# Kernel optimization log

Hardware: AMD Instinct MI355X
Metric: run time of the kernel (lower is better)

## Reference

```python
import jax, jax.numpy as jnp
import numpy as np
import math
from jax import lax

L = 30      # seq length (DyConv(30,30); fcblock in_dim 420 = 14*30)
D = 14      # d_model / channels
H = 8       # n_heads
E = D // H  # d_keys per head = 1 (torch integer division)
DK = H * E  # inner attention dim = 8
DFF = 50
TOPK = int(math.log(L))  # factor=1 -> 3
MA = 25     # Autoformer series_decomp moving-average kernel
EPS = 1e-5
B = 65536


def layer_norm(x, g, b):
    m = x.mean(-1, keepdims=True)
    v = ((x - m) ** 2).mean(-1, keepdims=True)
    return (x - m) / jnp.sqrt(v + EPS) * g + b


def series_decomp(x):
    # x: (B, L, D). Replicate-pad then moving average (kernel MA, stride 1).
    p = (MA - 1) // 2
    xp = jnp.concatenate([jnp.repeat(x[:, :1], p, axis=1), x, jnp.repeat(x[:, -1:], p, axis=1)], axis=1)
    cs = jnp.cumsum(xp, axis=1)
    cs = jnp.concatenate([jnp.zeros_like(cs[:, :1]), cs], axis=1)
    mean = (cs[:, MA:] - cs[:, :-MA]) / MA  # (B, L, D)
    return x - mean, mean


def _forward(x, W_emb, b_emb, Wq, bq, Wk, bk, Wv, bv, Wo, bo, W_ff1, W_ff2,
             g_norm, b_norm, W_dy, b_dy, channels, W1, b1, W2, b2, Wres, bres,
             g_ln, b_ln, W3, b3):
    Bn = x.shape[0]
    # --- Conv1d embedding: 14->14, kernel 3, padding 1 ---
    xc = x.transpose(0, 2, 1)  # (B, D, L)
    xc = lax.conv_general_dilated(xc, W_emb, (1,), ((1, 1),),
                                  dimension_numbers=("NCH", "OIH", "NCH")) + b_emb[None, :, None]
    x = xc.transpose(0, 2, 1)  # (B, L, D)
    # --- AutoCorrelation attention (eval mode: time_delay_agg_inference) ---
    q = (x @ Wq + bq).reshape(Bn, L, H, E).transpose(0, 2, 3, 1)  # (B,H,E,L)
    k = (x @ Wk + bk).reshape(Bn, L, H, E).transpose(0, 2, 3, 1)
    v = (x @ Wv + bv).reshape(Bn, L, H, E).transpose(0, 2, 3, 1)
    qf = jnp.fft.rfft(q, axis=-1)
    kf = jnp.fft.rfft(k, axis=-1)
    corr = jnp.fft.irfft(qf * jnp.conj(kf), n=L, axis=-1)  # (B,H,E,L)
    mean_value = corr.mean(axis=(1, 2))                    # (B,L)
    weights, delay = lax.top_k(mean_value, TOPK)           # (B,k)
    tmp_corr = jax.nn.softmax(weights, axis=-1)
    # circular gather at each top-k delay (== torch's doubled-values gather)
    idx = (jnp.arange(L)[None, None, :] + delay[:, :, None]) % L  # (B,k,L)
    idx_b = jnp.broadcast_to(idx[:, :, None, None, :], (Bn, TOPK, H, E, L))
    vk = jnp.broadcast_to(v[:, None], (Bn, TOPK, H, E, L))
    gathered = jnp.take_along_axis(vk, idx_b, axis=-1)            # (B,k,H,E,L)
    agg = jnp.einsum("bkhel,bk->bhel", gathered, tmp_corr)        # (B,H,E,L)
    new_x = agg.transpose(0, 3, 1, 2).reshape(Bn, L, DK) @ Wo + bo  # (B,L,D)
    # --- Autoformer EncoderLayer: decomp + 1x1-conv FFN + decomp; Encoder final norm ---
    x = x + new_x
    x, _ = series_decomp(x)
    y = jax.nn.gelu(x @ W_ff1, approximate=False) @ W_ff2  # conv1/conv2 are 1x1, bias=False
    x, _ = series_decomp(x + y)
    x = layer_norm(x, g_norm, b_norm)
    # --- DyConv: softmax adjacency over channels + linear over time ---
    xc = x.transpose(0, 2, 1)                 # (B, D, L)
    adj = jax.nn.softmax(channels, axis=-1)   # (D, D)
    h = xc @ W_dy + b_dy                      # linear over time dim
    dy = jax.nn.relu(jnp.einsum("ij,bjl->bil", adj, h))  # (B, D, L)
    f = dy.reshape(Bn, D * L)                 # (B, 420)
    # --- MLP head (eval mode: dropout = identity) ---
    hh = jax.nn.relu(f @ W1 + b1) @ W2 + b2
    out = layer_norm(hh + f @ Wres + bres, g_ln, b_ln)
    return out @ W3 + b3                      # (B, 1)


def setup_inputs():
    key = jax.random.key(0)
    ks = jax.random.split(key, 32)
    n = jax.random.normal
    s = 0.05
    return {
        "x": n(ks[0], (B, L, D), jnp.float32),
        "W_emb": n(ks[1], (D, D, 3), jnp.float32) * s,
        "b_emb": n(ks[2], (D,), jnp.float32) * s,
        "Wq": n(ks[3], (D, DK), jnp.float32) * s, "bq": n(ks[4], (DK,), jnp.float32) * s,
        "Wk": n(ks[5], (D, DK), jnp.float32) * s, "bk": n(ks[6], (DK,), jnp.float32) * s,
        "Wv": n(ks[7], (D, DK), jnp.float32) * s, "bv": n(ks[8], (DK,), jnp.float32) * s,
        "Wo": n(ks[9], (DK, D), jnp.float32) * s, "bo": n(ks[10], (D,), jnp.float32) * s,
        "W_ff1": n(ks[11], (D, DFF), jnp.float32) * s,
        "W_ff2": n(ks[12], (DFF, D), jnp.float32) * s,
        "g_norm": jnp.ones((D,), jnp.float32), "b_norm": jnp.zeros((D,), jnp.float32),
        "W_dy": n(ks[13], (L, L), jnp.float32) * s, "b_dy": n(ks[14], (L,), jnp.float32) * s,
        "channels": jax.random.uniform(ks[15], (D, D), jnp.float32),
        "W1": n(ks[16], (D * L, 256), jnp.float32) * s, "b1": n(ks[17], (256,), jnp.float32) * s,
        "W2": n(ks[18], (256, 64), jnp.float32) * s, "b2": n(ks[19], (64,), jnp.float32) * s,
        "Wres": n(ks[20], (D * L, 64), jnp.float32) * s, "bres": n(ks[21], (64,), jnp.float32) * s,
        "g_ln": jnp.ones((64,), jnp.float32), "b_ln": jnp.zeros((64,), jnp.float32),
        "W3": n(ks[22], (64, 1), jnp.float32) * s, "b3": n(ks[23], (1,), jnp.float32) * s,
    }


def reference(x, W_emb, b_emb, Wq, bq, Wk, bk, Wv, bv, Wo, bo, W_ff1, W_ff2,
              g_norm, b_norm, W_dy, b_dy, channels, W1, b1, W2, b2, Wres, bres,
              g_ln, b_ln, W3, b3):
    return _forward(x, W_emb, b_emb, Wq, bq, Wk, bk, Wv, bv, Wo, bo, W_ff1, W_ff2,
                    g_norm, b_norm, W_dy, b_dy, channels, W1, b1, W2, b2, Wres, bres,
                    g_ln, b_ln, W3, b3)
```

## Files before the change

### kernel.cpp

```cpp
#include <hip/hip_runtime.h>
#include <hip/hip_bf16.h>
#include <math.h>

#define LLEN 30
#define DMOD 14
#define NH 8
#define NFF 50
#define LN_EPS 1e-5f
#define K1P 448
#define NREC_W1 14336
#define NREC_WR 3584
#define NREC_W2 2048
#define NPREP_W (NREC_W1 + NREC_WR + NREC_W2)
#define NF1T 700
#define NEMT 588
#define NDYT 900

typedef unsigned short u16;
typedef unsigned int u32;
typedef __attribute__((ext_vector_type(8))) short s16x8;
typedef __attribute__((ext_vector_type(4))) float f32x4;

__device__ __forceinline__ float bflo(u32 v) {
  union { u32 u; float f; } w; w.u = v << 16; return w.f;
}
__device__ __forceinline__ u16 f2bf(float f) {
  union { float f; u32 u; } w; w.f = f;
  u32 x = w.u;
  x = (x + 0x7FFFu + ((x >> 16) & 1u)) >> 16;
  return (u16)x;
}
__device__ __forceinline__ u32 pk2(float lo, float hi) {
  return (u32)f2bf(lo) | ((u32)f2bf(hi) << 16);
}
__device__ __forceinline__ float2 f2fma(float2 a, float2 b, float2 c) {
  float2 r; r.x = fmaf(a.x, b.x, c.x); r.y = fmaf(a.y, b.y, c.y); return r;
}

__device__ __forceinline__ float gelu_fast(float a) {
  const float z  = fabsf(a) * 0.70710678118654752f;
  const float t  = __builtin_amdgcn_rcpf(1.f + 0.3275911f * z);
  const float p  = t * (0.254829592f + t * (-0.284496736f +
                   t * (1.421413741f + t * (-1.453152027f + t * 1.061405429f))));
  float e = 1.f - p * __expf(-z * z);
  e = copysignf(e, a);
  return 0.5f * a * (1.f + e);
}

__device__ __forceinline__ void decomp_row_lds(float* row) {
  float xv[30];
  const float2* r2 = (const float2*)row;
  #pragma unroll
  for (int j = 0; j < 15; ++j) { float2 w = r2[j]; xv[2*j] = w.x; xv[2*j+1] = w.y; }
  float2* w2 = (float2*)row;
  float ws = 13.f * xv[0];
  #pragma unroll
  for (int j = 1; j <= 12; ++j) ws += xv[j];
  float rprev = xv[0] - ws * (1.f / 25.f);
  #pragma unroll
  for (int jj = 1; jj < 30; ++jj) {
    const int hi = (jj + 12 > 29) ? 29 : jj + 12;
    const int lo = (jj - 13 < 0) ? 0 : jj - 13;
    ws += xv[hi] - xv[lo];
    const float r = xv[jj] - ws * (1.f / 25.f);
    if (jj & 1) { w2[jj >> 1] = make_float2(rprev, r); } else { rprev = r; }
  }
}

__global__ __launch_bounds__(64, 3) void fe_kernel(
    const float* __restrict__ x,
    const float* __restrict__ b_emb,
    const float* __restrict__ Wq, const float* __restrict__ bq,
    const float* __restrict__ Wk, const float* __restrict__ bk,
    const float* __restrict__ Wv, const float* __restrict__ bv,
    const float* __restrict__ Wo, const float* __restrict__ bo,
    const float* __restrict__ W_ff2,
    const float* __restrict__ g_norm, const float* __restrict__ b_norm,
    const float* __restrict__ b_dy,
    const float* __restrict__ channels,
    const float* __restrict__ wff1T, const float* __restrict__ wembT,
    const float* __restrict__ wdyT,
    u16* __restrict__ f_out, int Btot)
{
  const int t    = threadIdx.x;
  const int half = t >> 5;
  const int l    = t & 31;
  const int base = half << 5;
  const bool act = (l < LLEN);
  const int b    = blockIdx.x * 2 + half;
  const bool live = act && (b < Btot);

  __shared__ float pool[2][600];
  __shared__ float adjLDS[DMOD][16];
  __shared__ float MV[2][32];
  __shared__ float TW[2][4];
  __shared__ int   TD[2][4];

  float xr[DMOD];
  if (live) {
    const float2* xp2 = (const float2*)(x + (size_t)b * 420 + l * DMOD);
    #pragma unroll
    for (int j = 0; j < 7; ++j) { float2 v = xp2[j]; xr[2*j] = v.x; xr[2*j+1] = v.y; }
  } else {
    #pragma unroll
    for (int d = 0; d < DMOD; ++d) xr[d] = 0.f;
  }
  if (t < DMOD) {
    float row[DMOD]; float m = -1e30f;
    #pragma unroll
    for (int j = 0; j < DMOD; ++j) { row[j] = channels[t * DMOD + j]; m = fmaxf(m, row[j]); }
    float s = 0.f;
    #pragma unroll
    for (int j = 0; j < DMOD; ++j) { row[j] = __expf(row[j] - m); s += row[j]; }
    const float inv = 1.f / s;
    #pragma unroll
    for (int j = 0; j < DMOD; ++j) adjLDS[t][j] = row[j] * inv;
  }

  float2 xe2[7];
  {
    const float2* be2 = (const float2*)b_emb;
    #pragma unroll
    for (int o = 0; o < 7; ++o) xe2[o] = be2[o];
  }
  #pragma unroll
  for (int c = 0; c < DMOD; ++c) {
    float xm = __shfl(xr[c], t - 1);
    float xp = __shfl(xr[c], t + 1);
    xm = (l == 0) ? 0.f : xm;
    xp = (l >= LLEN - 1) ? 0.f : xp;
    const float xc = xr[c];
    const float2* w0  = (const float2*)(wembT + c * 42);
    const float2* w1p = (const float2*)(wembT + c * 42 + 14);
    const float2* w2p = (const float2*)(wembT + c * 42 + 28);
    const float2 m2 = make_float2(xm, xm);
    const float2 c2 = make_float2(xc, xc);
    const float2 p2 = make_float2(xp, xp);
    #pragma unroll
    for (int o = 0; o < 7; ++o)
      xe2[o] = f2fma(m2, w0[o], f2fma(c2, w1p[o], f2fma(p2, w2p[o], xe2[o])));
  }

  float2 q2[4], k2[4], v2[4];
  {
    const float2* bq2 = (const float2*)bq;
    const float2* bk2 = (const float2*)bk;
    const float2* bv2 = (const float2*)bv;
    #pragma unroll
    for (int jj = 0; jj < 4; ++jj) { q2[jj] = bq2[jj]; k2[jj] = bk2[jj]; v2[jj] = bv2[jj]; }
  }
  #pragma unroll
  for (int d = 0; d < DMOD; ++d) {
    const float e = (d & 1) ? xe2[d >> 1].y : xe2[d >> 1].x;
    const float2 e2 = make_float2(e, e);
    const float2* wq2 = (const float2*)(Wq + d * NH);
    const float2* wk2 = (const float2*)(Wk + d * NH);
    const float2* wv2 = (const float2*)(Wv + d * NH);
    #pragma unroll
    for (int jj = 0; jj < 4; ++jj) {
      q2[jj] = f2fma(e2, wq2[jj], q2[jj]);
      k2[jj] = f2fma(e2, wk2[jj], k2[jj]);
      v2[jj] = f2fma(e2, wv2[jj], v2[jj]);
    }
  }

  if (act) {
    float2* qr = (float2*)&pool[half][l * 10];
    qr[0] = q2[0]; qr[1] = q2[1]; qr[2] = q2[2]; qr[3] = q2[3];
    float2* kr = (float2*)&pool[half][300 + l * 10];
    kr[0] = k2[0]; kr[1] = k2[1]; kr[2] = k2[2]; kr[3] = k2[3];
  }
  __syncthreads();
  if (act) {
    float2 aa = make_float2(0.f, 0.f), ab = make_float2(0.f, 0.f);
    #pragma unroll 5
    for (int s = 0; s < LLEN; ++s) {
      int rq = l + s; if (rq >= LLEN) rq -= LLEN;
      const float2* qa = (const float2*)&pool[half][rq * 10];
      const float2* ka = (const float2*)&pool[half][300 + s * 10];
      aa = f2fma(qa[0], ka[0], aa); ab = f2fma(qa[1], ka[1], ab);
      aa = f2fma(qa[2], ka[2], aa); ab = f2fma(qa[3], ka[3], ab);
    }
    MV[half][l] = (aa.x + aa.y + ab.x + ab.y) * (1.f / NH);
  }
  __syncthreads();

  if (l == 0) {
    float v1 = -1e30f, v2v = -1e30f, v3 = -1e30f; int i1 = 0, i2 = 0, i3 = 0;
    for (int i = 0; i < LLEN; ++i) {
      const float vv = MV[half][i];
      if (vv > v1)       { v3 = v2v; i3 = i2; v2v = v1; i2 = i1; v1 = vv; i1 = i; }
      else if (vv > v2v) { v3 = v2v; i3 = i2; v2v = vv; i2 = i; }
      else if (vv > v3)  { v3 = vv; i3 = i; }
    }
    const float e2 = __expf(v2v - v1), e3 = __expf(v3 - v1);
    const float inv = 1.f / (1.f + e2 + e3);
    TW[half][0] = inv; TW[half][1] = e2 * inv; TW[half][2] = e3 * inv;
    TD[half][0] = i1; TD[half][1] = i2; TD[half][2] = i3;
  }
  __syncthreads();

  float agg[NH];
  #pragma unroll
  for (int h = 0; h < NH; ++h) agg[h] = 0.f;
  #pragma unroll
  for (int kk = 0; kk < 3; ++kk) {
    const float w = TW[half][kk];
    const int dd = TD[half][kk];
    int sidx = l + dd; if (sidx >= LLEN) sidx -= LLEN;
    const int src = base + sidx;
    #pragma unroll
    for (int h = 0; h < NH; ++h) {
      const float vh = (h & 1) ? v2[h >> 1].y : v2[h >> 1].x;
      agg[h] += w * __shfl(vh, src);
    }
  }

  {
    const float2* bo2 = (const float2*)bo;
    #pragma unroll
    for (int d2 = 0; d2 < 7; ++d2) {
      xe2[d2].x += bo2[d2].x; xe2[d2].y += bo2[d2].y;
    }
  }
  #pragma unroll
  for (int h = 0; h < NH; ++h) {
    const float2 ag = make_float2(agg[h], agg[h]);
    const float2* wo2 = (const float2*)(Wo + h * DMOD);
    #pragma unroll
    for (int d2 = 0; d2 < 7; ++d2) xe2[d2] = f2fma(ag, wo2[d2], xe2[d2]);
  }
  __syncthreads();

  if (act) {
    #pragma unroll
    for (int d = 0; d < DMOD; ++d)
      pool[half][d * LLEN + l] = (d & 1) ? xe2[d >> 1].y : xe2[d >> 1].x;
  }
  __syncthreads();
  if (l < DMOD) decomp_row_lds(&pool[half][l * LLEN]);
  __syncthreads();
  float2 s1p[7];
  if (act) {
    #pragma unroll
    for (int j = 0; j < 7; ++j)
      s1p[j] = make_float2(pool[half][(2 * j) * LLEN + l], pool[half][(2 * j + 1) * LLEN + l]);
  } else {
    #pragma unroll
    for (int j = 0; j < 7; ++j) s1p[j] = make_float2(0.f, 0.f);
  }
  __syncthreads();

  float2 y2[7];
  #pragma unroll
  for (int j = 0; j < 7; ++j) y2[j] = make_float2(0.f, 0.f);
  #pragma unroll 5
  for (int ff = 0; ff < NFF; ++ff) {
    const float2* w1r = (const float2*)(wff1T + ff * DMOD);
    float2 a2 = make_float2(0.f, 0.f), c2 = make_float2(0.f, 0.f);
    a2 = f2fma(s1p[0], w1r[0], a2); c2 = f2fma(s1p[1], w1r[1], c2);
    a2 = f2fma(s1p[2], w1r[2], a2); c2 = f2fma(s1p[3], w1r[3], c2);
    a2 = f2fma(s1p[4], w1r[4], a2); c2 = f2fma(s1p[5], w1r[5], c2);
    a2 = f2fma(s1p[6], w1r[6], a2);
    const float a = a2.x + a2.y + c2.x + c2.y;
    const float gl = gelu_fast(a);
    const float2 g2 = make_float2(gl, gl);
    const float2* w2r = (const float2*)(W_ff2 + ff * DMOD);
    #pragma unroll
    for (int j = 0; j < 7; ++j) y2[j] = f2fma(g2, w2r[j], y2[j]);
  }

  if (act) {
    #pragma unroll
    for (int j = 0; j < 7; ++j) {
      pool[half][(2 * j) * LLEN + l]     = s1p[j].x + y2[j].x;
      pool[half][(2 * j + 1) * LLEN + l] = s1p[j].y + y2[j].y;
    }
  }
  __syncthreads();
  if (l < DMOD) decomp_row_lds(&pool[half][l * LLEN]);
  __syncthreads();

  float2 ln2[7];
  if (act) {
    float s2v[DMOD];
    #pragma unroll
    for (int d = 0; d < DMOD; ++d) s2v[d] = pool[half][d * LLEN + l];
    float m = 0.f;
    #pragma unroll
    for (int d = 0; d < DMOD; ++d) m += s2v[d];
    m *= (1.f / DMOD);
    float va = 0.f;
    #pragma unroll
    for (int d = 0; d < DMOD; ++d) { const float z = s2v[d] - m; va += z * z; }
    va *= (1.f / DMOD);
    const float inv = rsqrtf(va + LN_EPS);
    #pragma unroll
    for (int j = 0; j < 7; ++j) {
      const float za = (s2v[2 * j] - m) * inv;
      const float zb = (s2v[2 * j + 1] - m) * inv;
      ln2[j] = make_float2(fmaf(za, g_norm[2 * j], b_norm[2 * j]),
                           fmaf(zb, g_norm[2 * j + 1], b_norm[2 * j + 1]));
    }
  } else {
    #pragma unroll
    for (int j = 0; j < 7; ++j) ln2[j] = make_float2(0.f, 0.f);
  }
  __syncthreads();

  float u[DMOD];
  #pragma unroll
  for (int i = 0; i < DMOD; ++i) {
    const float4* ar = (const float4*)&adjLDS[i][0];
    const float4 c0 = ar[0], c1 = ar[1], c2 = ar[2];
    const float2 c3 = ((const float2*)ar)[6];
    float2 ua = make_float2(0.f, 0.f), ub = make_float2(0.f, 0.f);
    ua = f2fma(make_float2(c0.x, c0.y), ln2[0], ua);
    ub = f2fma(make_float2(c0.z, c0.w), ln2[1], ub);
    ua = f2fma(make_float2(c1.x, c1.y), ln2[2], ua);
    ub = f2fma(make_float2(c1.z, c1.w), ln2[3], ub);
    ua = f2fma(make_float2(c2.x, c2.y), ln2[4], ua);
    ub = f2fma(make_float2(c2.z, c2.w), ln2[5], ub);
    ua = f2fma(c3, ln2[6], ua);
    u[i] = ua.x + ua.y + ub.x + ub.y;
  }
  if (act) {
    float4* ur = (float4*)&pool[half][l * 16];
    ur[0] = make_float4(u[0], u[1], u[2], u[3]);
    ur[1] = make_float4(u[4], u[5], u[6], u[7]);
    ur[2] = make_float4(u[8], u[9], u[10], u[11]);
    ((float2*)ur)[6] = make_float2(u[12], u[13]);
  }
  __syncthreads();

  if (live) {
    float2 acc2[7];
    #pragma unroll
    for (int j = 0; j < 7; ++j) acc2[j] = make_float2(0.f, 0.f);
    const float* wcol = wdyT + l * LLEN;
    #pragma unroll 5
    for (int lp = 0; lp < LLEN; ++lp) {
      const float wd = wcol[lp];
      const float2 w2v = make_float2(wd, wd);
      const float4* ur = (const float4*)&pool[half][lp * 16];
      const float4 a0 = ur[0], a1 = ur[1], a2 = ur[2];
      const float2 a3 = ((const float2*)ur)[6];
      acc2[0] = f2fma(w2v, make_float2(a0.x, a0.y), acc2[0]);
      acc2[1] = f2fma(w2v, make_float2(a0.z, a0.w), acc2[1]);
      acc2[2] = f2fma(w2v, make_float2(a1.x, a1.y), acc2[2]);
      acc2[3] = f2fma(w2v, make_float2(a1.z, a1.w), acc2[3]);
      acc2[4] = f2fma(w2v, make_float2(a2.x, a2.y), acc2[4]);
      acc2[5] = f2fma(w2v, make_float2(a2.z, a2.w), acc2[5]);
      acc2[6] = f2fma(w2v, a3, acc2[6]);
    }
    const float bd = b_dy[l];
    u16* fo = f_out + (size_t)b * K1P + l;
    #pragma unroll
    for (int i = 0; i < DMOD; ++i) {
      const float av = (i & 1) ? acc2[i >> 1].y : acc2[i >> 1].x;
      fo[i * LLEN] = f2bf(fmaxf(av + bd, 0.f));
    }
    if (l < 28) f_out[(size_t)b * K1P + 420 + l] = (u16)0;
  }
}

__global__ void prep_kernel(const float* __restrict__ W1,
                            const float* __restrict__ Wres,
                            const float* __restrict__ W2,
                            const float* __restrict__ W_ff1,
                            const float* __restrict__ W_emb,
                            const float* __restrict__ W_dy,
                            u16* __restrict__ w1s,
                            u16* __restrict__ wrh, u16* __restrict__ wrl,
                            u16* __restrict__ w2h, u16* __restrict__ w2l,
                            float* __restrict__ wff1T, float* __restrict__ wembT,
                            float* __restrict__ wdyT)
{
  const int idx = blockIdx.x * 256 + threadIdx.x;
  if (idx < NREC_W1) {
    const int n1 = idx & 255;
    const int cs = idx >> 8;
    const int k0 = cs * 8;
    union { u16 h[8]; uint4 q; } R;
    #pragma unroll
    for (int i = 0; i < 8; ++i) {
      const int k = k0 + i;
      const float w = (k < 420) ? W1[k * 256 + n1] : 0.f;
      R.h[i] = f2bf(w);
    }
    *((uint4*)(w1s + (size_t)idx * 8)) = R.q;
  } else if (idx < NREC_W1 + NREC_WR) {
    const int id = idx - NREC_W1;
    const int row = id & 63;
    const int cs = id >> 6;
    const int k0 = cs * 8;
    union { u16 h[8]; uint4 q; } Rh, Rl;
    #pragma unroll
    for (int i = 0; i < 8; ++i) {
      const int k = k0 + i;
      const float w = (k < 420) ? Wres[k * 64 + row] : 0.f;
      const u16 hh = f2bf(w);
      Rh.h[i] = hh;
      Rl.h[i] = f2bf(w - bflo((u32)hh));
    }
    *((uint4*)(wrh + (size_t)id * 8)) = Rh.q;
    *((uint4*)(wrl + (size_t)id * 8)) = Rl.q;
  } else if (idx < NPREP_W) {
    const int id = idx - NREC_W1 - NREC_WR;
    const int row = id & 63;
    const int cs = id >> 6;
    const int k0 = cs * 8;
    union { u16 h[8]; uint4 q; } Rh, Rl;
    #pragma unroll
    for (int i = 0; i < 8; ++i) {
      const float w = W2[(k0 + i) * 64 + row];
      const u16 hh = f2bf(w);
      Rh.h[i] = hh;
      Rl.h[i] = f2bf(w - bflo((u32)hh));
    }
    *((uint4*)(w2h + (size_t)id * 8)) = Rh.q;
    *((uint4*)(w2l + (size_t)id * 8)) = Rl.q;
  } else if (idx < NPREP_W + NF1T) {
    const int of = idx - NPREP_W;
    const int ff = of / DMOD;
    const int d  = of - ff * DMOD;
    wff1T[of] = W_ff1[d * NFF + ff];
  } else if (idx < NPREP_W + NF1T + NEMT) {
    const int of = idx - NPREP_W - NF1T;
    const int c  = of / 42;
    const int r  = of - c * 42;
    const int kk = r / DMOD;
    const int o  = r - kk * DMOD;
    wembT[of] = W_emb[o * 42 + c * 3 + kk];
  } else if (idx < NPREP_W + NF1T + NEMT + NDYT) {
    const int of = idx - NPREP_W - NF1T - NEMT;
    const int l  = of / LLEN;
    const int lp = of - l * LLEN;
    wdyT[of] = W_dy[lp * LLEN + l];
  }
}

__global__ __launch_bounds__(256, 2) void head_mfma(
    const u16* __restrict__ f, const u16* __restrict__ w1s,
    const u16* __restrict__ wrh, const u16* __restrict__ wrl,
    const u16* __restrict__ w2h, const u16* __restrict__ w2l,
    const float* __restrict__ b1, const float* __restrict__ b2,
    const float* __restrict__ bres, const float* __restrict__ g_ln,
    const float* __restrict__ b_ln, const float* __restrict__ W3,
    const float* __restrict__ b3, float* __restrict__ out, int Btot)
{
  const int t    = threadIdx.x;
  const int lane = t & 63;
  const int wv   = t >> 6;
  const int g    = lane >> 4;
  const int m    = lane & 15;
  const int samp = blockIdx.x * 64 + wv * 16 + m;
  const int srow = (samp < Btot) ? samp : (Btot - 1);

  __shared__ u16 wlds[19200];
  uint4* w4 = (uint4*)wlds;
  const int to = t + (t >> 6);

  s16x8 fr[14];
  const u16* fp = f + (size_t)srow * K1P + g * 8;
  #pragma unroll
  for (int c = 0; c < 14; ++c)
    fr[c] = *((const s16x8*)(fp + 32 * c));

  const f32x4 zero4 = {0.f, 0.f, 0.f, 0.f};
  const int rbase = g * 520 + m * 8;

  {
    const uint4 ra = ((const uint4*)wrh)[t];
    const uint4 rb = ((const uint4*)wrl)[t];
    w4[to] = ra; w4[272 + to] = rb;
  }
  __syncthreads();

  f32x4 ac3[4] = {zero4, zero4, zero4, zero4};
  #pragma unroll
  for (int c = 0; c < 14; ++c) {
    uint4 na, nb;
    if (c < 13) {
      na = ((const uint4*)wrh)[(c + 1) * 256 + t];
      nb = ((const uint4*)wrl)[(c + 1) * 256 + t];
    }
    #pragma unroll
    for (int nt = 0; nt < 4; ++nt) {
      const s16x8 ah = *(const s16x8*)&wlds[rbase + nt * 128];
      ac3[nt] = __builtin_amdgcn_mfma_f32_16x16x32_bf16(ah, fr[c], ac3[nt], 0, 0, 0);
    }
    #pragma unroll
    for (int nt = 0; nt < 4; ++nt) {
      const s16x8 al = *(const s16x8*)&wlds[2176 + rbase + nt * 128];
      ac3[nt] = __builtin_amdgcn_mfma_f32_16x16x32_bf16(al, fr[c], ac3[nt], 0, 0, 0);
    }
    __syncthreads();
    if (c < 13) { w4[to] = na; w4[272 + to] = nb; }
    __syncthreads();
  }

  f32x4 ac2[4] = {zero4, zero4, zero4, zero4};
  const int ap0 = ((g & 1) << 7) + (m << 2);
  const int ap1 = ap0 + 64;

  {
    #pragma unroll
    for (int i = 0; i < 7; ++i) {
      const int u = t + i * 256;
      const uint4 rv = ((const uint4*)w1s)[(u >> 5) * 256 + (u & 31)];
      w4[u + (u >> 5)] = rv;
    }
    const uint4 h2 = ((const uint4*)w2h)[t];
    const uint4 l2 = ((const uint4*)w2l)[t];
    w4[1856 + to] = h2;
    w4[1856 + 272 + to] = l2;
  }
  __syncthreads();

  #pragma unroll 1
  for (int j = 0; j < 8; ++j) {
    uint4 n1[7], nh2, nl2;
    if (j < 7) {
      #pragma unroll
      for (int i = 0; i < 7; ++i) {
        const int u = t + i * 256;
        n1[i] = ((const uint4*)w1s)[(u >> 5) * 256 + 32 * (j + 1) + (u & 31)];
      }
      nh2 = ((const uint4*)w2h)[(j + 1) * 256 + t];
      nl2 = ((const uint4*)w2l)[(j + 1) * 256 + t];
    }
    f32x4 ha0 = zero4, ha1 = zero4, hb0 = zero4, hb1 = zero4;
    #pragma unroll
    for (int c = 0; c < 14; c += 2) {
      const int A0 = (4 * c + g) * 264 + m * 8;
      const int A1 = (4 * (c + 1) + g) * 264 + m * 8;
      const s16x8 wa0 = *(const s16x8*)&wlds[A0];
      const s16x8 wb0 = *(const s16x8*)&wlds[A0 + 128];
      const s16x8 wa1 = *(const s16x8*)&wlds[A1];
      const s16x8 wb1 = *(const s16x8*)&wlds[A1 + 128];
      ha0 = __builtin_amdgcn_mfma_f32_16x16x32_bf16(wa0, fr[c], ha0, 0, 0, 0);
      hb0 = __builtin_amdgcn_mfma_f32_16x16x32_bf16(wb0, fr[c], hb0, 0, 0, 0);
      ha1 = __builtin_amdgcn_mfma_f32_16x16x32_bf16(wa1, fr[c + 1], ha1, 0, 0, 0);
      hb1 = __builtin_amdgcn_mfma_f32_16x16x32_bf16(wb1, fr[c + 1], hb1, 0, 0, 0);
    }
    const f32x4 ha = ha0 + ha1;
    const f32x4 hb = hb0 + hb1;
    const int f0 = 32 * j + 4 * g;
    const float H00 = fmaxf(ha[0] + b1[f0 + 0], 0.f);
    const float H01 = fmaxf(ha[1] + b1[f0 + 1], 0.f);
    const float H02 = fmaxf(ha[2] + b1[f0 + 2], 0.f);
    const float H03 = fmaxf(ha[3] + b1[f0 + 3], 0.f);
    const float H10 = fmaxf(hb[0] + b1[f0 + 16], 0.f);
    const float H11 = fmaxf(hb[1] + b1[f0 + 17], 0.f);
    const float H12 = fmaxf(hb[2] + b1[f0 + 18], 0.f);
    const float H13 = fmaxf(hb[3] + b1[f0 + 19], 0.f);
    const u32 PK00 = pk2(H00, H01), PK01 = pk2(H10, H11);
    const u32 PK10 = pk2(H02, H03), PK11 = pk2(H12, H13);
    union { u32 u[4]; s16x8 v; } bb;
    {
      const u32 r0 = (u32)__builtin_amdgcn_ds_bpermute(ap0, (int)PK00);
      const u32 r1 = (u32)__builtin_amdgcn_ds_bpermute(ap0, (int)PK01);
      bb.u[0] = (g & 2) ? r1 : r0;
    }
    {
      const u32 r0 = (u32)__builtin_amdgcn_ds_bpermute(ap0, (int)PK10);
      const u32 r1 = (u32)__builtin_amdgcn_ds_bpermute(ap0, (int)PK11);
      bb.u[1] = (g & 2) ? r1 : r0;
    }
    {
      const u32 r0 = (u32)__builtin_amdgcn_ds_bpermute(ap1, (int)PK00);
      const u32 r1 = (u32)__builtin_amdgcn_ds_bpermute(ap1, (int)PK01);
      bb.u[2] = (g & 2) ? r1 : r0;
    }
    {
      const u32 r0 = (u32)__builtin_amdgcn_ds_bpermute(ap1, (int)PK10);
      const u32 r1 = (u32)__builtin_amdgcn_ds_bpermute(ap1, (int)PK11);
      bb.u[3] = (g & 2) ? r1 : r0;
    }
    #pragma unroll
    for (int nt = 0; nt < 4; ++nt) {
      const s16x8 a2h = *(const s16x8*)&wlds[14848 + rbase + nt * 128];
      ac2[nt] = __builtin_amdgcn_mfma_f32_16x16x32_bf16(a2h, bb.v, ac2[nt], 0, 0, 0);
    }
    #pragma unroll
    for (int nt = 0; nt < 4; ++nt) {
      const s16x8 a2l = *(const s16x8*)&wlds[14848 + 2176 + rbase + nt * 128];
      ac2[nt] = __builtin_amdgcn_mfma_f32_16x16x32_bf16(a2l, bb.v, ac2[nt], 0, 0, 0);
    }
    __syncthreads();
    if (j < 7) {
      #pragma unroll
      for (int i = 0; i < 7; ++i) {
        const int u = t + i * 256;
        w4[u + (u >> 5)] = n1[i];
      }
      w4[1856 + to] = nh2;
      w4[1856 + 272 + to] = nl2;
    }
    __syncthreads();
  }

  float vals[4][4];
  float s1 = 0.f, sq = 0.f;
  #pragma unroll
  for (int nt = 0; nt < 4; ++nt) {
    #pragma unroll
    for (int r = 0; r < 4; ++r) {
      const int fe = 16 * nt + 4 * g + r;
      const float val = ac2[nt][r] + ac3[nt][r] + b2[fe] + bres[fe];
      vals[nt][r] = val; s1 += val; sq += val * val;
    }
  }
  s1 += __shfl_xor(s1, 16); s1 += __shfl_xor(s1, 32);
  sq += __shfl_xor(sq, 16); sq += __shfl_xor(sq, 32);
  const float mean = s1 * (1.f / 64.f);
  const float var  = sq * (1.f / 64.f) - mean * mean;
  const float inv  = rsqrtf(var + LN_EPS);
  float pr = 0.f;
  #pragma unroll
  for (int nt = 0; nt < 4; ++nt) {
    #pragma unroll
    for (int r = 0; r < 4; ++r) {
      const int fe = 16 * nt + 4 * g + r;
      const float n = (vals[nt][r] - mean) * inv * g_ln[fe] + b_ln[fe];
      pr += n * W3[fe];
    }
  }
  pr += __shfl_xor(pr, 16); pr += __shfl_xor(pr, 32);
  if (g == 0 && samp < Btot) out[samp] = pr + b3[0];
}

extern "C" void kernel_launch(void* const* d_in, const int* in_sizes, int n_in,
                              void* d_out, int out_size, void* d_ws, size_t ws_size,
                              hipStream_t stream) {
  const float* x        = (const float*)d_in[0];
  const float* W_emb    = (const float*)d_in[1];
  const float* b_emb    = (const float*)d_in[2];
  const float* Wq       = (const float*)d_in[3];
  const float* bq       = (const float*)d_in[4];
  const float* Wk       = (const float*)d_in[5];
  const float* bk       = (const float*)d_in[6];
  const float* Wv       = (const float*)d_in[7];
  const float* bv       = (const float*)d_in[8];
  const float* Wo       = (const float*)d_in[9];
  const float* bo       = (const float*)d_in[10];
  const float* W_ff1    = (const float*)d_in[11];
  const float* W_ff2    = (const float*)d_in[12];
  const float* g_norm   = (const float*)d_in[13];
  const float* b_norm   = (const float*)d_in[14];
  const float* W_dy     = (const float*)d_in[15];
  const float* b_dy     = (const float*)d_in[16];
  const float* channels = (const float*)d_in[17];
  const float* W1       = (const float*)d_in[18];
  const float* b1       = (const float*)d_in[19];
  const float* W2       = (const float*)d_in[20];
  const float* b2       = (const float*)d_in[21];
  const float* Wres     = (const float*)d_in[22];
  const float* bres     = (const float*)d_in[23];
  const float* g_ln     = (const float*)d_in[24];
  const float* b_ln     = (const float*)d_in[25];
  const float* W3       = (const float*)d_in[26];
  const float* b3       = (const float*)d_in[27];

  const int B = in_sizes[0] / (LLEN * DMOD);

  u16* fbuf = (u16*)d_ws;
  u16* w1s  = fbuf + (size_t)B * K1P;
  u16* wrh  = w1s + (size_t)NREC_W1 * 8;
  u16* wrl  = wrh + (size_t)NREC_WR * 8;
  u16* w2h  = wrl + (size_t)NREC_WR * 8;
  u16* w2l  = w2h + (size_t)NREC_W2 * 8;
  float* fw    = (float*)(w2l + (size_t)NREC_W2 * 8);
  float* wff1T = fw;
  float* wembT = fw + NF1T;
  float* wdyT  = fw + NF1T + NEMT;

  const int prep_tot = NPREP_W + NF1T + NEMT + NDYT;
  prep_kernel<<<(prep_tot + 255) / 256, 256, 0, stream>>>(
      W1, Wres, W2, W_ff1, W_emb, W_dy,
      w1s, wrh, wrl, w2h, w2l, wff1T, wembT, wdyT);

  const int nb_fe = (B + 1) / 2;
  fe_kernel<<<nb_fe, 64, 0, stream>>>(x, b_emb, Wq, bq, Wk, bk, Wv, bv, Wo, bo,
                                      W_ff2, g_norm, b_norm, b_dy, channels,
                                      wff1T, wembT, wdyT, fbuf, B);

  const int nb_h = (B + 63) / 64;
  head_mfma<<<nb_h, 256, 0, stream>>>(fbuf, w1s, wrh, wrl, w2h, w2l,
                                      b1, b2, bres, g_ln, b_ln, W3, b3,
                                      (float*)d_out, B);
}
```

Measured before the change: 522.5 us.

## Restructure head GEMM loops with async global-to-LDS double buffering

```diff
diff --git a/kernel.cpp b/kernel.cpp
--- a/kernel.cpp
+++ b/kernel.cpp
@@ -20,6 +20,11 @@
 typedef unsigned int u32;
 typedef __attribute__((ext_vector_type(8))) short s16x8;
 typedef __attribute__((ext_vector_type(4))) float f32x4;
+
+#define GLL16(gsrc, ldst) \
+  __builtin_amdgcn_global_load_lds( \
+      (const __attribute__((address_space(1))) unsigned int*)(gsrc), \
+      (__attribute__((address_space(3))) unsigned int*)(ldst), 16, 0, 0)
 
 __device__ __forceinline__ float bflo(u32 v) {
   union { u32 u; float f; } w; w.u = v << 16; return w.f;
@@ -457,9 +462,7 @@
   const int samp = blockIdx.x * 64 + wv * 16 + m;
   const int srow = (samp < Btot) ? samp : (Btot - 1);
 
-  __shared__ u16 wlds[19200];
-  uint4* w4 = (uint4*)wlds;
-  const int to = t + (t >> 6);
+  __shared__ __align__(16) u16 wlds[24576];
 
   s16x8 fr[14];
   const u16* fp = f + (size_t)srow * K1P + g * 8;
@@ -468,84 +471,66 @@
     fr[c] = *((const s16x8*)(fp + 32 * c));
 
   const f32x4 zero4 = {0.f, 0.f, 0.f, 0.f};
-  const int rbase = g * 520 + m * 8;
-
-  {
-    const uint4 ra = ((const uint4*)wrh)[t];
-    const uint4 rb = ((const uint4*)wrl)[t];
-    w4[to] = ra; w4[272 + to] = rb;
-  }
-  __syncthreads();
-
-  f32x4 ac3[4] = {zero4, zero4, zero4, zero4};
-  #pragma unroll
+
+  auto stage_chunk = [&](int c, int p) {
+    const int bb = p * 12288;
+    const u16* s1 = w1s + c * 8192 + wv * 2048 + lane * 8;
+    #pragma unroll
+    for (int i = 0; i < 4; ++i)
+      GLL16(s1 + i * 512, &wlds[bb + wv * 2048 + i * 512]);
+    GLL16(wrh + c * 2048 + wv * 512 + lane * 8, &wlds[bb + 8192 + wv * 512]);
+    GLL16(wrl + c * 2048 + wv * 512 + lane * 8, &wlds[bb + 10240 + wv * 512]);
+  };
+  auto stage_w2 = [&](int j, int r) {
+    GLL16(w2h + j * 2048 + wv * 512 + lane * 8, &wlds[r * 4096 + wv * 512]);
+    GLL16(w2l + j * 2048 + wv * 512 + lane * 8, &wlds[r * 4096 + 2048 + wv * 512]);
+  };
+
+  f32x4 hw1[16];
+  #pragma unroll
+  for (int nt = 0; nt < 16; ++nt) hw1[nt] = zero4;
+  f32x4 arh[4] = {zero4, zero4, zero4, zero4};
+  f32x4 arl[4] = {zero4, zero4, zero4, zero4};
+
+  stage_chunk(0, 0);
+  __syncthreads();
+
+  const int rb1 = g * 2048 + m * 8;
+  const int rbr = g * 512 + m * 8;
+  int pp = 0;
   for (int c = 0; c < 14; ++c) {
-    uint4 na, nb;
-    if (c < 13) {
-      na = ((const uint4*)wrh)[(c + 1) * 256 + t];
-      nb = ((const uint4*)wrl)[(c + 1) * 256 + t];
+    if (c < 13) stage_chunk(c + 1, pp ^ 1);
+    const int b0 = pp * 12288;
+    #pragma unroll
+    for (int nt = 0; nt < 16; ++nt) {
+      const s16x8 a = *(const s16x8*)&wlds[b0 + rb1 + nt * 128];
+      hw1[nt] = __builtin_amdgcn_mfma_f32_16x16x32_bf16(a, fr[c], hw1[nt], 0, 0, 0);
     }
     #pragma unroll
     for (int nt = 0; nt < 4; ++nt) {
-      const s16x8 ah = *(const s16x8*)&wlds[rbase + nt * 128];
-      ac3[nt] = __builtin_amdgcn_mfma_f32_16x16x32_bf16(ah, fr[c], ac3[nt], 0, 0, 0);
-    }
-    #pragma unroll
-    for (int nt = 0; nt < 4; ++nt) {
-      const s16x8 al = *(const s16x8*)&wlds[2176 + rbase + nt * 128];
-      ac3[nt] = __builtin_amdgcn_mfma_f32_16x16x32_bf16(al, fr[c], ac3[nt], 0, 0, 0);
+      const s16x8 ah = *(const s16x8*)&wlds[b0 + 8192 + rbr + nt * 128];
+      arh[nt] = __builtin_amdgcn_mfma_f32_16x16x32_bf16(ah, fr[c], arh[nt], 0, 0, 0);
+      const s16x8 al = *(const s16x8*)&wlds[b0 + 10240 + rbr + nt * 128];
+      arl[nt] = __builtin_amdgcn_mfma_f32_16x16x32_bf16(al, fr[c], arl[nt], 0, 0, 0);
     }
     __syncthreads();
-    if (c < 13) { w4[to] = na; w4[272 + to] = nb; }
-    __syncthreads();
-  }
-
-  f32x4 ac2[4] = {zero4, zero4, zero4, zero4};
+    pp ^= 1;
+  }
+
+  f32x4 a2hi[4] = {zero4, zero4, zero4, zero4};
+  f32x4 a2lo[4] = {zero4, zero4, zero4, zero4};
   const int ap0 = ((g & 1) << 7) + (m << 2);
   const int ap1 = ap0 + 64;
 
-  {
-    #pragma unroll
-    for (int i = 0; i < 7; ++i) {
-      const int u = t + i * 256;
-      const uint4 rv = ((const uint4*)w1s)[(u >> 5) * 256 + (u & 31)];
-      w4[u + (u >> 5)] = rv;
-    }
-    const uint4 h2 = ((const uint4*)w2h)[t];
-    const uint4 l2 = ((const uint4*)w2l)[t];
-    w4[1856 + to] = h2;
-    w4[1856 + 272 + to] = l2;
-  }
+  stage_w2(0, 0);
   __syncthreads();
 
   #pragma unroll 1
   for (int j = 0; j < 8; ++j) {
-    uint4 n1[7], nh2, nl2;
-    if (j < 7) {
-      #pragma unroll
-      for (int i = 0; i < 7; ++i) {
-        const int u = t + i * 256;
-        n1[i] = ((const uint4*)w1s)[(u >> 5) * 256 + 32 * (j + 1) + (u & 31)];
-      }
-      nh2 = ((const uint4*)w2h)[(j + 1) * 256 + t];
-      nl2 = ((const uint4*)w2l)[(j + 1) * 256 + t];
-    }
-    f32x4 ha0 = zero4, ha1 = zero4, hb0 = zero4, hb1 = zero4;
-    #pragma unroll
-    for (int c = 0; c < 14; c += 2) {
-      const int A0 = (4 * c + g) * 264 + m * 8;
-      const int A1 = (4 * (c + 1) + g) * 264 + m * 8;
-      const s16x8 wa0 = *(const s16x8*)&wlds[A0];
-      const s16x8 wb0 = *(const s16x8*)&wlds[A0 + 128];
-      const s16x8 wa1 = *(const s16x8*)&wlds[A1];
-      const s16x8 wb1 = *(const s16x8*)&wlds[A1 + 128];
-      ha0 = __builtin_amdgcn_mfma_f32_16x16x32_bf16(wa0, fr[c], ha0, 0, 0, 0);
-      hb0 = __builtin_amdgcn_mfma_f32_16x16x32_bf16(wb0, fr[c], hb0, 0, 0, 0);
-      ha1 = __builtin_amdgcn_mfma_f32_16x16x32_bf16(wa1, fr[c + 1], ha1, 0, 0, 0);
-      hb1 = __builtin_amdgcn_mfma_f32_16x16x32_bf16(wb1, fr[c + 1], hb1, 0, 0, 0);
-    }
-    const f32x4 ha = ha0 + ha1;
-    const f32x4 hb = hb0 + hb1;
+    if (j < 7) stage_w2(j + 1, (j + 1) & 1);
+    const int wb = (j & 1) * 4096;
+    const f32x4 ha = hw1[2 * j];
+    const f32x4 hb = hw1[2 * j + 1];
     const int f0 = 32 * j + 4 * g;
     const float H00 = fmaxf(ha[0] + b1[f0 + 0], 0.f);
     const float H01 = fmaxf(ha[1] + b1[f0 + 1], 0.f);
@@ -580,23 +565,10 @@
     }
     #pragma unroll
     for (int nt = 0; nt < 4; ++nt) {
-      const s16x8 a2h = *(const s16x8*)&wlds[14848 + rbase + nt * 128];
-      ac2[nt] = __builtin_amdgcn_mfma_f32_16x16x32_bf16(a2h, bb.v, ac2[nt], 0, 0, 0);
-    }
-    #pragma unroll
-    for (int nt = 0; nt < 4; ++nt) {
-      const s16x8 a2l = *(const s16x8*)&wlds[14848 + 2176 + rbase + nt * 128];
-      ac2[nt] = __builtin_amdgcn_mfma_f32_16x16x32_bf16(a2l, bb.v, ac2[nt], 0, 0, 0);
-    }
-    __syncthreads();
-    if (j < 7) {
-      #pragma unroll
-      for (int i = 0; i < 7; ++i) {
-        const int u = t + i * 256;
-        w4[u + (u >> 5)] = n1[i];
-      }
-      w4[1856 + to] = nh2;
-      w4[1856 + 272 + to] = nl2;
+      const s16x8 a2h = *(const s16x8*)&wlds[wb + rbr + nt * 128];
+      a2hi[nt] = __builtin_amdgcn_mfma_f32_16x16x32_bf16(a2h, bb.v, a2hi[nt], 0, 0, 0);
+      const s16x8 a2l = *(const s16x8*)&wlds[wb + 2048 + rbr + nt * 128];
+      a2lo[nt] = __builtin_amdgcn_mfma_f32_16x16x32_bf16(a2l, bb.v, a2lo[nt], 0, 0, 0);
     }
     __syncthreads();
   }
@@ -608,7 +580,8 @@
     #pragma unroll
     for (int r = 0; r < 4; ++r) {
       const int fe = 16 * nt + 4 * g + r;
-      const float val = ac2[nt][r] + ac3[nt][r] + b2[fe] + bres[fe];
+      const float val = a2hi[nt][r] + a2lo[nt][r] + arh[nt][r] + arl[nt][r]
+                      + b2[fe] + bres[fe];
       vals[nt][r] = val; s1 += val; sq += val * val;
     }
   }
```

Result: slower. 587.6 us (+12.5%).
